# Performance work log

Hardware: AMD Instinct MI355X
Metric: run time of the kernel (lower is better)

The kernel has to match this reference:

```python
import jax, jax.numpy as jnp
import numpy as np

# Llama-7B FFN up-proj quantized with HQQ 4-bit, group_size=64, axis=0
OUT, IN, GS = 11008, 4096, 64
G = OUT * IN // GS  # 704512 groups


def setup_inputs() -> dict:
    key = jax.random.key(0)
    k1, k2, k3, k4, k5 = jax.random.split(key, 5)
    # packed 4-bit weights: two nibbles per byte, shape [GS//2, G]
    W_q = jax.random.randint(k1, (GS // 2, G), 0, 256, dtype=jnp.int32)
    # per-group scale (meta['scale'] = 1/scale from quantize) and zero
    scale = jax.random.uniform(k2, (1, G), jnp.float32, minval=1e-3, maxval=1e-2)
    zero = jax.random.uniform(k3, (1, G), jnp.float32, minval=0.0, maxval=15.0)
    # decode-style activations: 8 sequences, 1 token each
    x = jax.random.normal(k4, (8, 1, IN), dtype=jnp.float32)
    bias = jax.random.normal(k5, (OUT,), dtype=jnp.float32) * 0.01
    return {"W_q": W_q, "scale": scale, "zero": zero, "x": x, "bias": bias}


def reference(W_q, scale, zero, x, bias):
    # BitPack.unpack_4bit_u8: high nibble rows stacked on low nibble rows
    hi = (W_q >> 4) & 0xF
    lo = W_q & 0xF
    W_q_p = jnp.concatenate([hi, lo], axis=0).astype(x.dtype)  # [GS, G]
    # Quantizer.dequantize: (W_q_p - zero) * scale, reshape to weight shape
    W_r = ((W_q_p - zero) * scale).reshape(OUT, IN)  # [out, in]
    # torch.nn.functional.linear(x, W_r, bias)
    return jnp.einsum('bsi,oi->bso', x, W_r) + bias
```

## Files before the change

kernel.cpp:

```cpp
#include <hip/hip_runtime.h>


#define OUT_ 11008
#define IN_ 4096
#define G_ 704512
#define OC_ 172
#define KS 4
#define KC (IN_ / KS)
#define ITERS (KC / 256)

__global__ __launch_bounds__(256, 4)
void hqq_gemv(const int* __restrict__ Wq, const float* __restrict__ scale,
              const float* __restrict__ zero, const float* __restrict__ x,
              float* __restrict__ ws) {
    __shared__ float s_lds[KC];
    __shared__ float z_lds[KC];
    __shared__ float x_lds[8 * KC];

    const int lane = threadIdx.x;
    const int ty   = threadIdx.y;
    const int tid  = ty * 64 + lane;
    const int oc   = blockIdx.y;
    const int ks   = blockIdx.z;
    const int rq0  = blockIdx.x * 8 + ty * 2;

    const int kbase = ks * KC;
    const long gb = (long)oc * IN_ + kbase;

    {
        const int off = tid * 4;
        *(float4*)(s_lds + off) = *(const float4*)(scale + gb + off);
        *(float4*)(z_lds + off) = *(const float4*)(zero + gb + off);
    }
#pragma unroll
    for (int r = 0; r < 8 * KC / 1024; ++r) {
        const int off = r * 1024 + tid * 4;
        const int b = off >> 10;
        const int k = off & (KC - 1);
        *(float4*)(x_lds + off) = *(const float4*)(x + b * IN_ + kbase + k);
    }

    const int* __restrict__ wqA = Wq + (long)rq0 * G_ + gb;
    const int* __restrict__ wqB = wqA + G_;
    int4 qA[ITERS], qB[ITERS];
#pragma unroll
    for (int it = 0; it < ITERS; ++it) {
        qA[it] = *(const int4*)(wqA + it * 256 + lane * 4);
        qB[it] = *(const int4*)(wqB + it * 256 + lane * 4);
    }

    __syncthreads();

    float acc[4][8];
#pragma unroll
    for (int r = 0; r < 4; ++r)
#pragma unroll
        for (int b = 0; b < 8; ++b) acc[r][b] = 0.f;

#pragma unroll
    for (int it = 0; it < ITERS; ++it) {
        const int i = it * 256 + lane * 4;
        const float4 s4 = *(const float4*)(s_lds + i);
        const float4 z4 = *(const float4*)(z_lds + i);
        const float ss[4] = {s4.x, s4.y, s4.z, s4.w};
        const float zs[4] = {-z4.x * s4.x, -z4.y * s4.y, -z4.z * s4.z, -z4.w * s4.w};
        const int qsA[4] = {qA[it].x, qA[it].y, qA[it].z, qA[it].w};
        const int qsB[4] = {qB[it].x, qB[it].y, qB[it].z, qB[it].w};

        float w[4][4];
#pragma unroll
        for (int j = 0; j < 4; ++j) {
            w[0][j] = fmaf((float)((qsA[j] >> 4) & 0xF), ss[j], zs[j]);
            w[1][j] = fmaf((float)( qsA[j]       & 0xF), ss[j], zs[j]);
            w[2][j] = fmaf((float)((qsB[j] >> 4) & 0xF), ss[j], zs[j]);
            w[3][j] = fmaf((float)( qsB[j]       & 0xF), ss[j], zs[j]);
        }
#pragma unroll
        for (int b = 0; b < 8; ++b) {
            const float4 xb = *(const float4*)(x_lds + b * KC + i);
#pragma unroll
            for (int r = 0; r < 4; ++r) {
                float a = acc[r][b];
                a = fmaf(xb.x, w[r][0], a);
                a = fmaf(xb.y, w[r][1], a);
                a = fmaf(xb.z, w[r][2], a);
                a = fmaf(xb.w, w[r][3], a);
                acc[r][b] = a;
            }
        }
    }

#pragma unroll
    for (int r = 0; r < 4; ++r)
#pragma unroll
        for (int b = 0; b < 8; ++b) {
            float v = acc[r][b];
#pragma unroll
            for (int off = 32; off > 0; off >>= 1)
                v += __shfl_down(v, off, 64);
            acc[r][b] = v;
        }

    if (lane == 0) {
        const int o[4] = {rq0 * OC_ + oc, (rq0 + 32) * OC_ + oc,
                          (rq0 + 1) * OC_ + oc, (rq0 + 33) * OC_ + oc};
        float* __restrict__ wp = ws + (long)ks * 8 * OUT_;
#pragma unroll
        for (int r = 0; r < 4; ++r)
#pragma unroll
            for (int b = 0; b < 8; ++b)
                wp[b * OUT_ + o[r]] = acc[r][b];
    }
}

__global__ void hqq_reduce(const float* __restrict__ ws,
                           const float* __restrict__ bias,
                           float* __restrict__ out) {
    const int t = blockIdx.x * 256 + threadIdx.x;
    if (t >= 8 * OUT_) return;
    const int o = t % OUT_;
    float v = bias[o];
#pragma unroll
    for (int k = 0; k < KS; ++k) v += ws[k * 8 * OUT_ + t];
    out[t] = v;
}

extern "C" void kernel_launch(void* const* d_in, const int* in_sizes, int n_in,
                              void* d_out, int out_size, void* d_ws, size_t ws_size,
                              hipStream_t stream) {
    const int*   Wq    = (const int*)d_in[0];
    const float* scale = (const float*)d_in[1];
    const float* zero  = (const float*)d_in[2];
    const float* x     = (const float*)d_in[3];
    const float* bias  = (const float*)d_in[4];
    float* out = (float*)d_out;
    float* ws  = (float*)d_ws;

    dim3 grid(4, OC_, KS);
    dim3 block(64, 4);
    hqq_gemv<<<grid, block, 0, stream>>>(Wq, scale, zero, x, ws);
    hqq_reduce<<<(8 * OUT_ + 255) / 256, 256, 0, stream>>>(ws, bias, out);
}
```

Baseline: 152.5 us.

## Process four packed rows per wave with rolling two-deep weight prefetch

Each wave now handles four packed rows (eight output rows) instead of two, so every scale/zero and x value read from LDS is reused across twice as many outputs. The grid is halved along x to match. Weight loads change from loading every iteration up front to a two-stage rolling prefetch (current plus next), which keeps register use in check despite the doubled accumulator tile. Occupancy drops: the launch-bounds hint goes from 4 to 3 blocks, and there are half as many blocks in flight, so less parallelism is available to hide memory latency.

After: 157.9 us. 1.04x slower.

```diff
diff --git a/kernel.cpp b/kernel.cpp
--- a/kernel.cpp
+++ b/kernel.cpp
@@ -7,9 +7,9 @@
 #define OC_ 172
 #define KS 4
 #define KC (IN_ / KS)
-#define ITERS (KC / 256)
+#define NIT (KC / 256)
 
-__global__ __launch_bounds__(256, 4)
+__global__ __launch_bounds__(256, 3)
 void hqq_gemv(const int* __restrict__ Wq, const float* __restrict__ scale,
               const float* __restrict__ zero, const float* __restrict__ x,
               float* __restrict__ ws) {
@@ -22,10 +22,19 @@
     const int tid  = ty * 64 + lane;
     const int oc   = blockIdx.y;
     const int ks   = blockIdx.z;
-    const int rq0  = blockIdx.x * 8 + ty * 2;
+    const int rq0  = blockIdx.x * 16 + ty * 4;
 
     const int kbase = ks * KC;
     const long gb = (long)oc * IN_ + kbase;
+    const int i0 = lane * 4;
+
+    const int* __restrict__ wq0 = Wq + (long)rq0 * G_ + gb;
+
+    int4 qc[4], qn[4];
+#pragma unroll
+    for (int r = 0; r < 4; ++r) qc[r] = *(const int4*)(wq0 + (long)r * G_ + i0);
+#pragma unroll
+    for (int r = 0; r < 4; ++r) qn[r] = *(const int4*)(wq0 + (long)r * G_ + i0 + 256);
 
     {
         const int off = tid * 4;
@@ -33,53 +42,56 @@
         *(float4*)(z_lds + off) = *(const float4*)(zero + gb + off);
     }
 #pragma unroll
-    for (int r = 0; r < 8 * KC / 1024; ++r) {
+    for (int r = 0; r < 8; ++r) {
         const int off = r * 1024 + tid * 4;
         const int b = off >> 10;
         const int k = off & (KC - 1);
         *(float4*)(x_lds + off) = *(const float4*)(x + b * IN_ + kbase + k);
     }
 
-    const int* __restrict__ wqA = Wq + (long)rq0 * G_ + gb;
-    const int* __restrict__ wqB = wqA + G_;
-    int4 qA[ITERS], qB[ITERS];
-#pragma unroll
-    for (int it = 0; it < ITERS; ++it) {
-        qA[it] = *(const int4*)(wqA + it * 256 + lane * 4);
-        qB[it] = *(const int4*)(wqB + it * 256 + lane * 4);
-    }
-
     __syncthreads();
 
-    float acc[4][8];
+    float acc[8][8];
 #pragma unroll
-    for (int r = 0; r < 4; ++r)
+    for (int r = 0; r < 8; ++r)
 #pragma unroll
         for (int b = 0; b < 8; ++b) acc[r][b] = 0.f;
 
 #pragma unroll
-    for (int it = 0; it < ITERS; ++it) {
-        const int i = it * 256 + lane * 4;
+    for (int it = 0; it < NIT; ++it) {
+        const int i = it * 256 + i0;
+
+        int4 q[4];
+#pragma unroll
+        for (int r = 0; r < 4; ++r) q[r] = qc[r];
+#pragma unroll
+        for (int r = 0; r < 4; ++r) qc[r] = qn[r];
+        if (it + 2 < NIT) {
+#pragma unroll
+            for (int r = 0; r < 4; ++r)
+                qn[r] = *(const int4*)(wq0 + (long)r * G_ + i + 512);
+        }
+
         const float4 s4 = *(const float4*)(s_lds + i);
         const float4 z4 = *(const float4*)(z_lds + i);
         const float ss[4] = {s4.x, s4.y, s4.z, s4.w};
         const float zs[4] = {-z4.x * s4.x, -z4.y * s4.y, -z4.z * s4.z, -z4.w * s4.w};
-        const int qsA[4] = {qA[it].x, qA[it].y, qA[it].z, qA[it].w};
-        const int qsB[4] = {qB[it].x, qB[it].y, qB[it].z, qB[it].w};
 
-        float w[4][4];
+        float w[8][4];
 #pragma unroll
-        for (int j = 0; j < 4; ++j) {
-            w[0][j] = fmaf((float)((qsA[j] >> 4) & 0xF), ss[j], zs[j]);
-            w[1][j] = fmaf((float)( qsA[j]       & 0xF), ss[j], zs[j]);
-            w[2][j] = fmaf((float)((qsB[j] >> 4) & 0xF), ss[j], zs[j]);
-            w[3][j] = fmaf((float)( qsB[j]       & 0xF), ss[j], zs[j]);
+        for (int rr = 0; rr < 4; ++rr) {
+            const int qs[4] = {q[rr].x, q[rr].y, q[rr].z, q[rr].w};
+#pragma unroll
+            for (int j = 0; j < 4; ++j) {
+                w[rr * 2 + 0][j] = fmaf((float)((qs[j] >> 4) & 0xF), ss[j], zs[j]);
+                w[rr * 2 + 1][j] = fmaf((float)( qs[j]       & 0xF), ss[j], zs[j]);
+            }
         }
 #pragma unroll
         for (int b = 0; b < 8; ++b) {
             const float4 xb = *(const float4*)(x_lds + b * KC + i);
 #pragma unroll
-            for (int r = 0; r < 4; ++r) {
+            for (int r = 0; r < 8; ++r) {
                 float a = acc[r][b];
                 a = fmaf(xb.x, w[r][0], a);
                 a = fmaf(xb.y, w[r][1], a);
@@ -91,7 +103,7 @@
     }
 
 #pragma unroll
-    for (int r = 0; r < 4; ++r)
+    for (int r = 0; r < 8; ++r)
 #pragma unroll
         for (int b = 0; b < 8; ++b) {
             float v = acc[r][b];
@@ -102,14 +114,17 @@
         }
 
     if (lane == 0) {
-        const int o[4] = {rq0 * OC_ + oc, (rq0 + 32) * OC_ + oc,
-                          (rq0 + 1) * OC_ + oc, (rq0 + 33) * OC_ + oc};
         float* __restrict__ wp = ws + (long)ks * 8 * OUT_;
 #pragma unroll
-        for (int r = 0; r < 4; ++r)
+        for (int rr = 0; rr < 4; ++rr) {
+            const int o_hi = (rq0 + rr) * OC_ + oc;
+            const int o_lo = (rq0 + rr + 32) * OC_ + oc;
 #pragma unroll
-            for (int b = 0; b < 8; ++b)
-                wp[b * OUT_ + o[r]] = acc[r][b];
+            for (int b = 0; b < 8; ++b) {
+                wp[b * OUT_ + o_hi] = acc[rr * 2 + 0][b];
+                wp[b * OUT_ + o_lo] = acc[rr * 2 + 1][b];
+            }
+        }
     }
 }
 
@@ -136,7 +151,7 @@
     float* out = (float*)d_out;
     float* ws  = (float*)d_ws;
 
-    dim3 grid(4, OC_, KS);
+    dim3 grid(2, OC_, KS);
     dim3 block(64, 4);
     hqq_gemv<<<grid, block, 0, stream>>>(Wq, scale, zero, x, ws);
     hqq_reduce<<<(8 * OUT_ + 255) / 256, 256, 0, stream>>>(ws, bias, out);
```
